# Kernel tuning notes

Hardware: AMD Instinct MI355X
Metric: run time of the kernel (lower is better)

The kernel has to match this reference:

```python
import jax, jax.numpy as jnp
import numpy as np

D = 512; H = 8; DK = 64; DFF = 512 * 8 // 3; NL = 3; WIN = 128
B = 4; L = 2048
VOCAB = 157; TE = 192


def _silu(x):
    return x * jax.nn.sigmoid(x)


def _ln(x, w, b):
    m = x.mean(-1, keepdims=True)
    v = ((x - m) ** 2).mean(-1, keepdims=True)
    return (x - m) / jnp.sqrt(v + 1e-5) * w + b


def _rms(x, w):
    return x / jnp.sqrt((x * x).mean(-1, keepdims=True) + 1.1920929e-7) * w


def _rope(t):
    # t: [B,H,L,DK]; rotary dim == DK (interleaved-pair convention of rotary-embedding-torch)
    Lq = t.shape[-2]
    inv = 1.0 / (10000.0 ** (jnp.arange(0, DK, 2, dtype=jnp.float32) / DK))
    ang = jnp.arange(Lq, dtype=jnp.float32)[:, None] * inv  # [L, DK/2]
    cos, sin = jnp.cos(ang), jnp.sin(ang)
    x1, x2 = t[..., ::2], t[..., 1::2]
    out = jnp.stack([x1 * cos - x2 * sin, x1 * sin + x2 * cos], axis=-1)
    return out.reshape(t.shape)


def _local_attn(h, qkv_w, ow, ob):
    Bq, Lq, _ = h.shape
    qkv = (h @ qkv_w.T).reshape(Bq, Lq, H, DK, 3)  # einops '(h d c)' ordering
    q = jnp.transpose(qkv[..., 0], (0, 2, 1, 3))
    k = jnp.transpose(qkv[..., 1], (0, 2, 1, 3))
    v = jnp.transpose(qkv[..., 2], (0, 2, 1, 3))
    q = _rope(q); k = _rope(k)
    nb = Lq // WIN
    qb = q.reshape(Bq, H, nb, WIN, DK)
    kb = k.reshape(Bq, H, nb, WIN, DK)
    vb = v.reshape(Bq, H, nb, WIN, DK)
    kp = jnp.concatenate([jnp.zeros_like(kb[:, :, :1]), kb[:, :, :-1]], axis=2)
    vp = jnp.concatenate([jnp.zeros_like(vb[:, :, :1]), vb[:, :, :-1]], axis=2)
    kc = jnp.concatenate([kp, kb], axis=3)  # [B,H,nb,2W,DK]
    vc = jnp.concatenate([vp, vb], axis=3)
    s = jnp.einsum('bhnqd,bhnkd->bhnqk', qb, kc) / np.float32(np.sqrt(DK))
    i = jnp.arange(WIN)[:, None]
    j = jnp.arange(2 * WIN)[None, :]
    band = (j >= i) & (j <= i + WIN)  # [W,2W]
    blk = jnp.arange(nb)[:, None, None]
    valid = band[None] & ((blk > 0) | (j[None] >= WIN))  # [nb,W,2W]
    s = jnp.where(valid[None, None], s, jnp.float32(-1e30))
    a = jax.nn.softmax(s, axis=-1)
    o = jnp.einsum('bhnqk,bhnkd->bhnqd', a, vc).reshape(Bq, H, Lq, DK)
    o = jnp.transpose(o, (0, 2, 1, 3)).reshape(Bq, Lq, D)
    return o @ ow.T + ob


def _net(x, emb, reg_w, reg_b, br_w, br_b, sh_w, sh_b, inst_w, inst_b, enc_ln_w, enc_ln_b,
         qkv_w, out_w, out_b, w1_w, w1_b, w3_w, w3_b, w2_w, w2_b, n1_w, n2_w,
         head_ln_w, head_ln_b, head_w, head_b):
    reg = x[..., 1:65].astype(jnp.float32)
    sh = x[..., 65:257].astype(jnp.float32)
    br = x[..., 257:289].astype(jnp.float32)
    te = emb[x[..., 0]]
    cat = jnp.concatenate([te, reg @ reg_w.T + reg_b, br @ br_w.T + br_b, sh @ sh_w.T + sh_b], axis=-1)
    h = _silu(cat) @ inst_w.T + inst_b
    h = _silu(_ln(h, enc_ln_w, enc_ln_b))
    for l in range(NL):
        h = h + _local_attn(_rms(h, n1_w[l]), qkv_w[l], out_w[l], out_b[l])
        h2 = _rms(h, n2_w[l])
        h = h + (_silu(h2 @ w1_w[l].T + w1_b[l]) * (h2 @ w3_w[l].T + w3_b[l])) @ w2_w[l].T + w2_b[l]
    y = _silu(_ln(h, head_ln_w, head_ln_b)) @ head_w.T + head_b  # [B,L,31]
    fc_log = y[..., 0:11]
    fc_reg = jax.nn.softplus(y[..., 11])
    ec_log = y[..., 12:23]
    ec_reg = jax.nn.softplus(y[..., 23])
    bm_log = y[..., 24]
    ic_log = y[..., 25:28]
    dc_log = y[..., 28:31]
    bm = jax.nn.sigmoid(bm_log)
    ic = jax.nn.softmax(ic_log, axis=-1)
    dc = jax.nn.softmax(dc_log, axis=-1)
    fc_pred = jnp.argmax(fc_log, axis=-1)
    fetch = jnp.where(fc_pred < 10, (fc_pred + 1).astype(jnp.float32), fc_reg)
    ec_pred = jnp.argmax(ec_log, axis=-1)
    execc = jnp.where(ec_pred < 10, (ec_pred + 1).astype(jnp.float32), ec_reg)
    # pack all task outputs into one [B,L,40] array
    return jnp.concatenate([
        fetch[..., None], fc_log, fc_reg[..., None],
        execc[..., None], ec_log, ec_reg[..., None],
        bm[..., None], ic, dc,
        bm_log[..., None], ic_log, dc_log], axis=-1)


def setup_inputs() -> dict:
    key = jax.random.key(0)
    ks = iter(jax.random.split(key, 64))
    g = lambda shape, s=0.02: (jax.random.normal(next(ks), shape, dtype=jnp.float32) * s)
    inp = {}
    inp['x'] = jax.random.randint(next(ks), (B, L, 289), 0, VOCAB, dtype=jnp.int64)
    inp['emb'] = g((VOCAB, TE), 1.0)
    inp['reg_w'] = g((TE, 64)); inp['reg_b'] = jnp.zeros((TE,), jnp.float32)
    inp['br_w'] = g((TE, 32)); inp['br_b'] = jnp.zeros((TE,), jnp.float32)
    inp['sh_w'] = g((TE, 192)); inp['sh_b'] = jnp.zeros((TE,), jnp.float32)
    inp['inst_w'] = g((D, 4 * TE)); inp['inst_b'] = jnp.zeros((D,), jnp.float32)
    inp['enc_ln_w'] = jnp.ones((D,), jnp.float32); inp['enc_ln_b'] = jnp.zeros((D,), jnp.float32)
    inp['qkv_w'] = g((NL, 3 * D, D))
    inp['out_w'] = g((NL, D, D)); inp['out_b'] = jnp.zeros((NL, D), jnp.float32)
    inp['w1_w'] = g((NL, DFF, D)); inp['w1_b'] = jnp.zeros((NL, DFF), jnp.float32)
    inp['w3_w'] = g((NL, DFF, D)); inp['w3_b'] = jnp.zeros((NL, DFF), jnp.float32)
    inp['w2_w'] = g((NL, D, DFF)); inp['w2_b'] = jnp.zeros((NL, D), jnp.float32)
    inp['n1_w'] = jnp.ones((NL, D), jnp.float32)
    inp['n2_w'] = jnp.ones((NL, D), jnp.float32)
    inp['head_ln_w'] = jnp.ones((D,), jnp.float32); inp['head_ln_b'] = jnp.zeros((D,), jnp.float32)
    inp['head_w'] = g((31, D)); inp['head_b'] = jnp.zeros((31,), jnp.float32)
    return inp


def reference(x, emb, reg_w, reg_b, br_w, br_b, sh_w, sh_b, inst_w, inst_b, enc_ln_w, enc_ln_b,
              qkv_w, out_w, out_b, w1_w, w1_b, w3_w, w3_b, w2_w, w2_b, n1_w, n2_w,
              head_ln_w, head_ln_b, head_w, head_b):
    return _net(x, emb, reg_w, reg_b, br_w, br_b, sh_w, sh_b, inst_w, inst_b, enc_ln_w, enc_ln_b,
                qkv_w, out_w, out_b, w1_w, w1_b, w3_w, w3_b, w2_w, w2_b, n1_w, n2_w,
                head_ln_w, head_ln_b, head_w, head_b)
```

## Files before the change

### kernel.cpp

```cpp
#include <hip/hip_runtime.h>
#include <hip/hip_bf16.h>
#include <math.h>

#define T_TOK 8192
#define DMODEL 512
#define NHEAD 8
#define TEDIM 192
#define DFF 1365
#define DFFP 1408
#define KP2 1376
#define NLAYER 3
#define WINSZ 128
#define NBLK 16
#define LSEQ 2048
#define BATCH 4

typedef unsigned short ushort_t;
typedef __bf16 bf16x8 __attribute__((ext_vector_type(8)));
typedef float f32x4 __attribute__((ext_vector_type(4)));
typedef float f32x16 __attribute__((ext_vector_type(16)));

__device__ __forceinline__ float silu_f(float x) { return x / (1.0f + expf(-x)); }
__device__ __forceinline__ float softplus_f(float x) {
    return (x > 20.0f) ? x : log1pf(expf(x));
}

__device__ __forceinline__ ushort_t f2u(float x) {
    __hip_bfloat16 b = __float2bfloat16(x);
    return *reinterpret_cast<ushort_t*>(&b);
}
__device__ __forceinline__ float u2f(ushort_t u) {
    __hip_bfloat16 b = *reinterpret_cast<__hip_bfloat16*>(&u);
    return __bfloat162float(b);
}
__device__ __forceinline__ void split2(float x, ushort_t& hi, ushort_t& lo) {
    hi = f2u(x);
    lo = f2u(x - u2f(hi));
}

__device__ __forceinline__ void gl_lds16(const ushort_t* g, ushort_t* l) {
    __builtin_amdgcn_global_load_lds(
        (const __attribute__((address_space(1))) unsigned int*)g,
        (__attribute__((address_space(3))) unsigned int*)l, 16, 0, 0);
}

__global__ __launch_bounds__(256)
void rope_kernel(float* __restrict__ ct, float* __restrict__ st) {
    int idx = blockIdx.x * 256 + threadIdx.x;
    int tok = idx >> 5, p = idx & 31;
    float invf = powf(10000.0f, -(float)p * (1.0f / 32.0f));
    float sn, cs;
    sincosf((float)tok * invf, &sn, &cs);
    ct[idx] = cs;
    st[idx] = sn;
}

__global__ __launch_bounds__(256)
void splitw_kernel(const float* __restrict__ W, ushort_t* __restrict__ W2,
                   int N, int K, int Kp) {
    int n = blockIdx.y;
    int k = blockIdx.x * 256 + threadIdx.x;
    if (k >= Kp) return;
    float v = (n < N && k < K) ? W[(size_t)n * K + k] : 0.0f;
    ushort_t hi, lo;
    split2(v, hi, lo);
    W2[(size_t)n * (2 * Kp) + k] = hi;
    W2[(size_t)n * (2 * Kp) + Kp + k] = lo;
}

__global__ __launch_bounds__(256)
void splitw_qkv_kernel(const float* __restrict__ W, ushort_t* __restrict__ W2) {
    int l = blockIdx.z;
    int rr = blockIdx.y;
    int k = blockIdx.x * 256 + threadIdx.x;
    int h = rr / 192, rem = rr % 192;
    int dk = rem / 3, which = rem % 3;
    int rp = which * 512 + h * 64 + dk;
    float v = W[((size_t)l * 1536 + rr) * 512 + k];
    ushort_t hi, lo;
    split2(v, hi, lo);
    W2[((size_t)l * 1536 + rp) * 1024 + k] = hi;
    W2[((size_t)l * 1536 + rp) * 1024 + 512 + k] = lo;
}

__global__ __launch_bounds__(256)
void splitw_ffn(const float* __restrict__ w1, const float* __restrict__ w3,
                ushort_t* __restrict__ W1s, ushort_t* __restrict__ W3s) {
    int rr = blockIdx.y;
    int k = blockIdx.x * 256 + threadIdx.x;
    int lyr = rr / DFFP, n = rr % DFFP;
    bool ok = (n < DFF);
    float v1 = ok ? w1[((size_t)lyr * DFF + n) * 512 + k] : 0.0f;
    float v3 = ok ? w3[((size_t)lyr * DFF + n) * 512 + k] : 0.0f;
    ushort_t hi, lo;
    split2(v1, hi, lo);
    W1s[(size_t)rr * 1024 + k] = hi;
    W1s[(size_t)rr * 1024 + 512 + k] = lo;
    split2(v3, hi, lo);
    W3s[(size_t)rr * 1024 + k] = hi;
    W3s[(size_t)rr * 1024 + 512 + k] = lo;
}

__global__ __launch_bounds__(256)
void splitw_w2(const float* __restrict__ W, ushort_t* __restrict__ W2) {
    int rr = blockIdx.y;
    int k = blockIdx.x * 256 + threadIdx.x;
    if (k >= KP2) return;
    int lyr = rr >> 9, n = rr & 511;
    float v = (k < DFF) ? W[((size_t)lyr * 512 + n) * DFF + k] : 0.0f;
    ushort_t hi, lo;
    split2(v, hi, lo);
    W2[(size_t)rr * (2 * KP2) + k] = hi;
    W2[(size_t)rr * (2 * KP2) + KP2 + k] = lo;
}

__global__ __launch_bounds__(256)
void build_encw(const float* __restrict__ reg_w, const float* __restrict__ reg_b,
                const float* __restrict__ br_w, const float* __restrict__ br_b,
                const float* __restrict__ sh_w, const float* __restrict__ sh_b,
                ushort_t* __restrict__ Wc2, float* __restrict__ bc) {
    int n = blockIdx.x;
    int tid = threadIdx.x;
    for (int k = tid; k < 288; k += 256) {
        float v = 0.0f;
        if (n < 192) {
            if (k < 64) v = reg_w[(size_t)n * 64 + k];
        } else if (n < 384) {
            if (k >= 256) v = br_w[(size_t)(n - 192) * 32 + (k - 256)];
        } else if (n < 576) {
            if (k >= 64 && k < 256) v = sh_w[(size_t)(n - 384) * 192 + (k - 64)];
        }
        ushort_t hi, lo;
        split2(v, hi, lo);
        Wc2[(size_t)n * 576 + k] = hi;
        Wc2[(size_t)n * 576 + 288 + k] = lo;
    }
    if (tid == 0) {
        float b = 0.0f;
        if (n < 192) b = reg_b[n];
        else if (n < 384) b = br_b[n - 192];
        else if (n < 576) b = sh_b[n - 384];
        bc[n] = b;
    }
}

__global__ __launch_bounds__(256)
void prep_tok(const int* __restrict__ x, const float* __restrict__ emb,
              ushort_t* __restrict__ X2, ushort_t* __restrict__ cat2) {
    int tok = blockIdx.x;
    int tid = threadIdx.x;
    const int* xp = x + (size_t)tok * 289;
    for (int k = tid; k < 288; k += 256) {
        X2[(size_t)tok * 576 + k] = f2u((float)xp[1 + k]);
        X2[(size_t)tok * 576 + 288 + k] = 0;
    }
    int tokid = xp[0];
    for (int c = tid; c < 192; c += 256) {
        float v = silu_f(emb[(size_t)tokid * TEDIM + c]);
        ushort_t hi, lo;
        split2(v, hi, lo);
        cat2[(size_t)tok * 1536 + c] = hi;
        cat2[(size_t)tok * 1536 + 768 + c] = lo;
    }
}


#define MFMA32(a, b, c) __builtin_amdgcn_mfma_f32_32x32x16_bf16(a, b, c, 0, 0, 0)

__global__ __launch_bounds__(256)
void gemm3_kernel(const ushort_t* __restrict__ A2, int rsA,
                  const ushort_t* __restrict__ B2, int rsB,
                  const float* __restrict__ bias,
                  const float* __restrict__ res,
                  float* __restrict__ Cf, int rsC, int Kp) {
    __shared__ __align__(16) ushort_t lds[4 * 4096];
    const int tid = threadIdx.x;
    const int bm = blockIdx.x * 128, bn = blockIdx.y * 128;
    const int w = tid >> 6, l = tid & 63;
    const int wm = (w & 1) * 64, wn = (w >> 1) * 64;

    f32x16 acc[2][2];
    #pragma unroll
    for (int i = 0; i < 2; ++i)
        #pragma unroll
        for (int j = 0; j < 2; ++j)
            #pragma unroll
            for (int r = 0; r < 16; ++r) acc[i][j][r] = 0.0f;

    const int r0 = tid >> 2;
    const int k8 = (((tid & 3) - (tid >> 3)) & 3) * 8;
    const ushort_t* gA0 = A2 + (size_t)(bm + r0) * rsA + k8;
    const ushort_t* gA1 = A2 + (size_t)(bm + 64 + r0) * rsA + k8;
    const ushort_t* gB0 = B2 + (size_t)(bn + r0) * rsB + k8;
    const ushort_t* gB1 = B2 + (size_t)(bn + 64 + r0) * rsB + k8;
    ushort_t* l0 = lds + tid * 8;
    ushort_t* l1 = lds + 2048 + tid * 8;

    const int ar = l & 31, qh = l >> 5;

    for (int kt = 0; kt < Kp; kt += 32) {
        gl_lds16(gA0 + kt, l0);
        gl_lds16(gA1 + kt, l1);
        gl_lds16(gA0 + kt + Kp, l0 + 4096);
        gl_lds16(gA1 + kt + Kp, l1 + 4096);
        gl_lds16(gB0 + kt, l0 + 8192);
        gl_lds16(gB1 + kt, l1 + 8192);
        gl_lds16(gB0 + kt + Kp, l0 + 12288);
        gl_lds16(gB1 + kt + Kp, l1 + 12288);
        __syncthreads();

        #pragma unroll
        for (int kh = 0; kh < 2; ++kh) {
            const int kq = kh * 2 + qh;
            bf16x8 ah[2], al_[2], bh[2], bl[2];
            #pragma unroll
            for (int i = 0; i < 2; ++i) {
                int row = wm + i * 32 + ar;
                int ba = row * 32 + (((kq + (row >> 1)) & 3) * 8);
                ah[i]  = *(const bf16x8*)&lds[ba];
                al_[i] = *(const bf16x8*)&lds[4096 + ba];
            }
            #pragma unroll
            for (int j = 0; j < 2; ++j) {
                int row = wn + j * 32 + ar;
                int bb = row * 32 + (((kq + (row >> 1)) & 3) * 8);
                bh[j] = *(const bf16x8*)&lds[8192 + bb];
                bl[j] = *(const bf16x8*)&lds[12288 + bb];
            }
            #pragma unroll
            for (int i = 0; i < 2; ++i)
                #pragma unroll
                for (int j = 0; j < 2; ++j) {
                    acc[i][j] = MFMA32(ah[i], bh[j], acc[i][j]);
                    acc[i][j] = MFMA32(ah[i], bl[j], acc[i][j]);
                    acc[i][j] = MFMA32(al_[i], bh[j], acc[i][j]);
                }
        }
        __syncthreads();
    }

    const int ec = l & 31, rb = (l >> 5) * 4;
    #pragma unroll
    for (int i = 0; i < 2; ++i)
        #pragma unroll
        for (int j = 0; j < 2; ++j) {
            int gn = bn + wn + j * 32 + ec;
            float bv = bias ? bias[gn] : 0.0f;
            #pragma unroll
            for (int r = 0; r < 16; ++r) {
                int gm = bm + wm + i * 32 + rb + (r & 3) + 8 * (r >> 2);
                float v = acc[i][j][r] + bv;
                if (res) v += res[(size_t)gm * rsC + gn];
                Cf[(size_t)gm * rsC + gn] = v;
            }
        }
}

__global__ __launch_bounds__(256)
void gemm3_enc(const ushort_t* __restrict__ A2, const ushort_t* __restrict__ B2,
               const float* __restrict__ bc, ushort_t* __restrict__ cat2) {
    __shared__ __align__(16) ushort_t lds[4 * 4096];
    const int tid = threadIdx.x;
    const int bm = blockIdx.x * 128, bn = blockIdx.y * 128;
    const int w = tid >> 6, l = tid & 63;
    const int wm = (w & 1) * 64, wn = (w >> 1) * 64;
    const int Kp = 288;

    f32x16 acc[2][2];
    #pragma unroll
    for (int i = 0; i < 2; ++i)
        #pragma unroll
        for (int j = 0; j < 2; ++j)
            #pragma unroll
            for (int r = 0; r < 16; ++r) acc[i][j][r] = 0.0f;

    const int r0 = tid >> 2;
    const int k8 = (((tid & 3) - (tid >> 3)) & 3) * 8;
    const ushort_t* gA0 = A2 + (size_t)(bm + r0) * 576 + k8;
    const ushort_t* gA1 = A2 + (size_t)(bm + 64 + r0) * 576 + k8;
    const ushort_t* gB0 = B2 + (size_t)(bn + r0) * 576 + k8;
    const ushort_t* gB1 = B2 + (size_t)(bn + 64 + r0) * 576 + k8;
    ushort_t* l0 = lds + tid * 8;
    ushort_t* l1 = lds + 2048 + tid * 8;
    const int ar = l & 31, qh = l >> 5;

    for (int kt = 0; kt < Kp; kt += 32) {
        gl_lds16(gA0 + kt, l0);
        gl_lds16(gA1 + kt, l1);
        gl_lds16(gA0 + kt + Kp, l0 + 4096);
        gl_lds16(gA1 + kt + Kp, l1 + 4096);
        gl_lds16(gB0 + kt, l0 + 8192);
        gl_lds16(gB1 + kt, l1 + 8192);
        gl_lds16(gB0 + kt + Kp, l0 + 12288);
        gl_lds16(gB1 + kt + Kp, l1 + 12288);
        __syncthreads();
        #pragma unroll
        for (int kh = 0; kh < 2; ++kh) {
            const int kq = kh * 2 + qh;
            bf16x8 ah[2], al_[2], bh[2], bl[2];
            #pragma unroll
            for (int i = 0; i < 2; ++i) {
                int row = wm + i * 32 + ar;
                int ba = row * 32 + (((kq + (row >> 1)) & 3) * 8);
                ah[i]  = *(const bf16x8*)&lds[ba];
                al_[i] = *(const bf16x8*)&lds[4096 + ba];
            }
            #pragma unroll
            for (int j = 0; j < 2; ++j) {
                int row = wn + j * 32 + ar;
                int bb = row * 32 + (((kq + (row >> 1)) & 3) * 8);
                bh[j] = *(const bf16x8*)&lds[8192 + bb];
                bl[j] = *(const bf16x8*)&lds[12288 + bb];
            }
            #pragma unroll
            for (int i = 0; i < 2; ++i)
                #pragma unroll
                for (int j = 0; j < 2; ++j) {
                    acc[i][j] = MFMA32(ah[i], bh[j], acc[i][j]);
                    acc[i][j] = MFMA32(ah[i], bl[j], acc[i][j]);
                    acc[i][j] = MFMA32(al_[i], bh[j], acc[i][j]);
                }
        }
        __syncthreads();
    }

    const int ec = l & 31, rb = (l >> 5) * 4;
    #pragma unroll
    for (int i = 0; i < 2; ++i)
        #pragma unroll
        for (int j = 0; j < 2; ++j) {
            int gn = bn + wn + j * 32 + ec;
            if (gn < 576) {
                float bv = bc[gn];
                #pragma unroll
                for (int r = 0; r < 16; ++r) {
                    int gm = bm + wm + i * 32 + rb + (r & 3) + 8 * (r >> 2);
                    float v = silu_f(acc[i][j][r] + bv);
                    ushort_t hi, lo;
                    split2(v, hi, lo);
                    cat2[(size_t)gm * 1536 + 192 + gn] = hi;
                    cat2[(size_t)gm * 1536 + 960 + gn] = lo;
                }
            }
        }
}

__global__ __launch_bounds__(256)
void gemm_glu3(const ushort_t* __restrict__ A2,
               const ushort_t* __restrict__ W1, const ushort_t* __restrict__ W3,
               const float* __restrict__ b1, const float* __restrict__ b3,
               ushort_t* __restrict__ C2) {
    __shared__ __align__(16) ushort_t lds[6 * 4096];
    const int tid = threadIdx.x;
    const int bm = blockIdx.x * 128, bn = blockIdx.y * 128;
    const int w = tid >> 6, l = tid & 63;
    const int wm = (w & 1) * 64, wn = (w >> 1) * 64;
    const int Kp = 512;

    f32x16 acc1[2][2], acc3[2][2];
    #pragma unroll
    for (int i = 0; i < 2; ++i)
        #pragma unroll
        for (int j = 0; j < 2; ++j)
            #pragma unroll
            for (int r = 0; r < 16; ++r) { acc1[i][j][r] = 0.0f; acc3[i][j][r] = 0.0f; }

    const int r0 = tid >> 2;
    const int k8 = (((tid & 3) - (tid >> 3)) & 3) * 8;
    const ushort_t* gA0 = A2 + (size_t)(bm + r0) * 1024 + k8;
    const ushort_t* gA1 = A2 + (size_t)(bm + 64 + r0) * 1024 + k8;
    const ushort_t* g10 = W1 + (size_t)(bn + r0) * 1024 + k8;
    const ushort_t* g11 = W1 + (size_t)(bn + 64 + r0) * 1024 + k8;
    const ushort_t* g30 = W3 + (size_t)(bn + r0) * 1024 + k8;
    const ushort_t* g31 = W3 + (size_t)(bn + 64 + r0) * 1024 + k8;
    ushort_t* l0 = lds + tid * 8;
    ushort_t* l1 = lds + 2048 + tid * 8;
    const int ar = l & 31, qh = l >> 5;

    for (int kt = 0; kt < Kp; kt += 32) {
        gl_lds16(gA0 + kt, l0);
        gl_lds16(gA1 + kt, l1);
        gl_lds16(gA0 + kt + Kp, l0 + 4096);
        gl_lds16(gA1 + kt + Kp, l1 + 4096);
        gl_lds16(g10 + kt, l0 + 8192);
        gl_lds16(g11 + kt, l1 + 8192);
        gl_lds16(g10 + kt + Kp, l0 + 12288);
        gl_lds16(g11 + kt + Kp, l1 + 12288);
        gl_lds16(g30 + kt, l0 + 16384);
        gl_lds16(g31 + kt, l1 + 16384);
        gl_lds16(g30 + kt + Kp, l0 + 20480);
        gl_lds16(g31 + kt + Kp, l1 + 20480);
        __syncthreads();

        #pragma unroll
        for (int kh = 0; kh < 2; ++kh) {
            const int kq = kh * 2 + qh;
            bf16x8 ah[2], al_[2];
            #pragma unroll
            for (int i = 0; i < 2; ++i) {
                int row = wm + i * 32 + ar;
                int ba = row * 32 + (((kq + (row >> 1)) & 3) * 8);
                ah[i]  = *(const bf16x8*)&lds[ba];
                al_[i] = *(const bf16x8*)&lds[4096 + ba];
            }
            #pragma unroll
            for (int j = 0; j < 2; ++j) {
                int row = wn + j * 32 + ar;
                int bb = row * 32 + (((kq + (row >> 1)) & 3) * 8);
                bf16x8 w1h = *(const bf16x8*)&lds[8192 + bb];
                bf16x8 w1l = *(const bf16x8*)&lds[12288 + bb];
                bf16x8 w3h = *(const bf16x8*)&lds[16384 + bb];
                bf16x8 w3l = *(const bf16x8*)&lds[20480 + bb];
                #pragma unroll
                for (int i = 0; i < 2; ++i) {
                    acc1[i][j] = MFMA32(ah[i], w1h, acc1[i][j]);
                    acc1[i][j] = MFMA32(ah[i], w1l, acc1[i][j]);
                    acc1[i][j] = MFMA32(al_[i], w1h, acc1[i][j]);
                    acc3[i][j] = MFMA32(ah[i], w3h, acc3[i][j]);
                    acc3[i][j] = MFMA32(ah[i], w3l, acc3[i][j]);
                    acc3[i][j] = MFMA32(al_[i], w3h, acc3[i][j]);
                }
            }
        }
        __syncthreads();
    }

    const int ec = l & 31, rb = (l >> 5) * 4;
    #pragma unroll
    for (int i = 0; i < 2; ++i)
        #pragma unroll
        for (int j = 0; j < 2; ++j) {
            int gn = bn + wn + j * 32 + ec;
            if (gn < KP2) {
                float bv1 = (gn < DFF) ? b1[gn] : 0.0f;
                float bv3 = (gn < DFF) ? b3[gn] : 0.0f;
                #pragma unroll
                for (int r = 0; r < 16; ++r) {
                    int gm = bm + wm + i * 32 + rb + (r & 3) + 8 * (r >> 2);
                    float g = silu_f(acc1[i][j][r] + bv1) * (acc3[i][j][r] + bv3);
                    ushort_t hi, lo;
                    split2(g, hi, lo);
                    C2[(size_t)gm * (2 * KP2) + gn] = hi;
                    C2[(size_t)gm * (2 * KP2) + KP2 + gn] = lo;
                }
            }
        }
}

__global__ __launch_bounds__(256)
void rms_kernel(const float* __restrict__ h, const float* __restrict__ w,
                ushort_t* __restrict__ out2) {
    int wid = threadIdx.x >> 6, lane = threadIdx.x & 63;
    int t = blockIdx.x * 4 + wid;
    const float* hp = h + (size_t)t * 512;
    float xv[8];
    float ss = 0.0f;
    #pragma unroll
    for (int u = 0; u < 8; ++u) { xv[u] = hp[u * 64 + lane]; ss += xv[u] * xv[u]; }
    #pragma unroll
    for (int off = 32; off > 0; off >>= 1) ss += __shfl_xor(ss, off, 64);
    float inv = rsqrtf(ss * (1.0f / 512.0f) + 1.1920929e-07f);
    ushort_t* op = out2 + (size_t)t * 1024;
    #pragma unroll
    for (int u = 0; u < 8; ++u) {
        ushort_t hi, lo;
        split2(xv[u] * inv * w[u * 64 + lane], hi, lo);
        op[u * 64 + lane] = hi;
        op[512 + u * 64 + lane] = lo;
    }
}

__global__ __launch_bounds__(256)
void ln_silu_kernel(const float* __restrict__ h, const float* __restrict__ w,
                    const float* __restrict__ b, float* __restrict__ out) {
    int wid = threadIdx.x >> 6, lane = threadIdx.x & 63;
    int t = blockIdx.x * 4 + wid;
    const float* hp = h + (size_t)t * 512;
    float xv[8];
    float s = 0.0f;
    #pragma unroll
    for (int u = 0; u < 8; ++u) { xv[u] = hp[u * 64 + lane]; s += xv[u]; }
    #pragma unroll
    for (int off = 32; off > 0; off >>= 1) s += __shfl_xor(s, off, 64);
    float m = s * (1.0f / 512.0f);
    float v = 0.0f;
    #pragma unroll
    for (int u = 0; u < 8; ++u) { xv[u] -= m; v += xv[u] * xv[u]; }
    #pragma unroll
    for (int off = 32; off > 0; off >>= 1) v += __shfl_xor(v, off, 64);
    float inv = rsqrtf(v * (1.0f / 512.0f) + 1e-5f);
    float* op = out + (size_t)t * 512;
    #pragma unroll
    for (int u = 0; u < 8; ++u)
        op[u * 64 + lane] = silu_f(xv[u] * inv * w[u * 64 + lane] + b[u * 64 + lane]);
}

__global__ __launch_bounds__(256)
void attn_kernel(const float* __restrict__ qkv, const float* __restrict__ ct,
                 const float* __restrict__ st, ushort_t* __restrict__ attn2) {
    __shared__ __align__(16) ushort_t Khi[32 * 64], Klo[32 * 64];
    __shared__ __align__(16) ushort_t Vthi[64 * 32], Vtlo[64 * 32];
    __shared__ __align__(16) ushort_t Phi[128 * 32], Plo[128 * 32];
    const int nb = blockIdx.x, head = blockIdx.y, b = blockIdx.z;
    const int tid = threadIdx.x;
    const int w = tid >> 6, lane = tid & 63;
    const int quad = lane >> 4, lc = lane & 15;

    bf16x8 qhi[2][2], qlo[2][2];
    #pragma unroll
    for (int i = 0; i < 2; ++i) {
        int qtok = nb * 128 + w * 32 + i * 16 + lc;
        const float* qp = qkv + ((size_t)(b * LSEQ + qtok)) * 1536 + head * 64;
        #pragma unroll
        for (int s = 0; s < 2; ++s) {
            float4 a = *(const float4*)&qp[s * 32 + quad * 8];
            float4 bq = *(const float4*)&qp[s * 32 + quad * 8 + 4];
            float4 c4 = *(const float4*)&ct[qtok * 32 + s * 16 + quad * 4];
            float4 s4 = *(const float4*)&st[qtok * 32 + s * 16 + quad * 4];
            float e[8];
            e[0] = (a.x * c4.x - a.y * s4.x) * 0.125f;
            e[1] = (a.x * s4.x + a.y * c4.x) * 0.125f;
            e[2] = (a.z * c4.y - a.w * s4.y) * 0.125f;
            e[3] = (a.z * s4.y + a.w * c4.y) * 0.125f;
            e[4] = (bq.x * c4.z - bq.y * s4.z) * 0.125f;
            e[5] = (bq.x * s4.z + bq.y * c4.z) * 0.125f;
            e[6] = (bq.z * c4.w - bq.w * s4.w) * 0.125f;
            e[7] = (bq.z * s4.w + bq.w * c4.w) * 0.125f;
            union { bf16x8 v; ushort_t u[8]; } hh, ll;
            #pragma unroll
            for (int d = 0; d < 8; ++d) split2(e[d], hh.u[d], ll.u[d]);
            qhi[i][s] = hh.v;
            qlo[i][s] = ll.v;
        }
    }

    f32x4 acc[2][4];
    float mrun[2][4], lrun[2][4];
    #pragma unroll
    for (int i = 0; i < 2; ++i) {
        #pragma unroll
        for (int j = 0; j < 4; ++j) acc[i][j] = (f32x4){0.f, 0.f, 0.f, 0.f};
        #pragma unroll
        for (int r = 0; r < 4; ++r) { mrun[i][r] = -1e30f; lrun[i][r] = 0.0f; }
    }

    const int c0 = (nb == 0) ? 4 : 0;
    for (int c = c0; c < 8; ++c) {
        {
            int key = tid >> 3, g = tid & 7;
            int ktok = nb * 128 - 128 + c * 32 + key;
            const float* kp = qkv + ((size_t)(b * LSEQ + ktok)) * 1536 + 512 + head * 64 + g * 8;
            float4 a = *(const float4*)kp;
            float4 bq = *(const float4*)(kp + 4);
            float4 c4 = *(const float4*)&ct[ktok * 32 + g * 4];
            float4 s4 = *(const float4*)&st[ktok * 32 + g * 4];
            float e[8];
            e[0] = a.x * c4.x - a.y * s4.x;
            e[1] = a.x * s4.x + a.y * c4.x;
            e[2] = a.z * c4.y - a.w * s4.y;
            e[3] = a.z * s4.y + a.w * c4.y;
            e[4] = bq.x * c4.z - bq.y * s4.z;
            e[5] = bq.x * s4.z + bq.y * c4.z;
            e[6] = bq.z * c4.w - bq.w * s4.w;
            e[7] = bq.z * s4.w + bq.w * c4.w;
            union { bf16x8 v; ushort_t u[8]; } hh, ll;
            #pragma unroll
            for (int d = 0; d < 8; ++d) split2(e[d], hh.u[d], ll.u[d]);
            int sg = g ^ (key & 7);
            *(bf16x8*)&Khi[key * 64 + sg * 8] = hh.v;
            *(bf16x8*)&Klo[key * 64 + sg * 8] = ll.v;

            const float* vp = kp + 512;
            float4 va = *(const float4*)vp;
            float4 vb = *(const float4*)(vp + 4);
            float ve[8] = {va.x, va.y, va.z, va.w, vb.x, vb.y, vb.z, vb.w};
            int kg = key >> 3, k7 = key & 7;
            #pragma unroll
            for (int d = 0; d < 8; ++d) {
                ushort_t vh, vl;
                split2(ve[d], vh, vl);
                int dim = g * 8 + d;
                int addr = dim * 32 + (((kg + (dim >> 1)) & 3) * 8) + k7;
                Vthi[addr] = vh;
                Vtlo[addr] = vl;
            }
        }
        __syncthreads();

        f32x4 sf[2][2];
        #pragma unroll
        for (int i = 0; i < 2; ++i)
            #pragma unroll
            for (int t = 0; t < 2; ++t) sf[i][t] = (f32x4){0.f, 0.f, 0.f, 0.f};
        #pragma unroll
        for (int t = 0; t < 2; ++t) {
            #pragma unroll
            for (int s = 0; s < 2; ++s) {
                int row = t * 16 + lc;
                int sg = (s * 4 + quad) ^ (row & 7);
                bf16x8 kh = *(const bf16x8*)&Khi[row * 64 + sg * 8];
                bf16x8 kl = *(const bf16x8*)&Klo[row * 64 + sg * 8];
                #pragma unroll
                for (int i = 0; i < 2; ++i) {
                    sf[i][t] = __builtin_amdgcn_mfma_f32_16x16x32_bf16(qhi[i][s], kh, sf[i][t], 0, 0, 0);
                    sf[i][t] = __builtin_amdgcn_mfma_f32_16x16x32_bf16(qhi[i][s], kl, sf[i][t], 0, 0, 0);
                    sf[i][t] = __builtin_amdgcn_mfma_f32_16x16x32_bf16(qlo[i][s], kh, sf[i][t], 0, 0, 0);
                }
            }
        }

        #pragma unroll
        for (int i = 0; i < 2; ++i) {
            #pragma unroll
            for (int r = 0; r < 4; ++r) {
                int qq = w * 32 + i * 16 + quad * 4 + r;
                float rm = -1e30f;
                #pragma unroll
                for (int t = 0; t < 2; ++t) {
                    int key = c * 32 + t * 16 + lc;
                    bool valid = (key >= qq) && (key <= qq + 128) && (nb > 0 || key >= 128);
                    float sv = valid ? sf[i][t][r] : -1e30f;
                    sf[i][t][r] = sv;
                    rm = fmaxf(rm, sv);
                }
                #pragma unroll
                for (int xm = 1; xm < 16; xm <<= 1)
                    rm = fmaxf(rm, __shfl_xor(rm, xm, 64));
                float mn = fmaxf(mrun[i][r], rm);
                float alpha = __expf(mrun[i][r] - mn);
                lrun[i][r] *= alpha;
                #pragma unroll
                for (int j = 0; j < 4; ++j) acc[i][j][r] *= alpha;
                float rs = 0.0f;
                #pragma unroll
                for (int t = 0; t < 2; ++t) {
                    int key = c * 32 + t * 16 + lc;
                    bool valid = (key >= qq) && (key <= qq + 128) && (nb > 0 || key >= 128);
                    float p = valid ? __expf(sf[i][t][r] - mn) : 0.0f;
                    rs += p;
                    ushort_t ph, pl;
                    split2(p, ph, pl);
                    int col = t * 16 + lc;
                    int addr = qq * 32 + ((((col >> 3) + (qq >> 1)) & 3) * 8) + (col & 7);
                    Phi[addr] = ph;
                    Plo[addr] = pl;
                }
                #pragma unroll
                for (int xm = 1; xm < 16; xm <<= 1)
                    rs += __shfl_xor(rs, xm, 64);
                lrun[i][r] += rs;
                mrun[i][r] = mn;
            }
        }

        bf16x8 ph[2], pl[2];
        #pragma unroll
        for (int i = 0; i < 2; ++i) {
            int row = w * 32 + i * 16 + lc;
            int sg = (quad + (row >> 1)) & 3;
            ph[i] = *(const bf16x8*)&Phi[row * 32 + sg * 8];
            pl[i] = *(const bf16x8*)&Plo[row * 32 + sg * 8];
        }
        #pragma unroll
        for (int j = 0; j < 4; ++j) {
            int dim = j * 16 + lc;
            int sg = (quad + (dim >> 1)) & 3;
            bf16x8 vh = *(const bf16x8*)&Vthi[dim * 32 + sg * 8];
            bf16x8 vl = *(const bf16x8*)&Vtlo[dim * 32 + sg * 8];
            #pragma unroll
            for (int i = 0; i < 2; ++i) {
                acc[i][j] = __builtin_amdgcn_mfma_f32_16x16x32_bf16(ph[i], vh, acc[i][j], 0, 0, 0);
                acc[i][j] = __builtin_amdgcn_mfma_f32_16x16x32_bf16(ph[i], vl, acc[i][j], 0, 0, 0);
                acc[i][j] = __builtin_amdgcn_mfma_f32_16x16x32_bf16(pl[i], vh, acc[i][j], 0, 0, 0);
            }
        }
        __syncthreads();
    }

    #pragma unroll
    for (int i = 0; i < 2; ++i) {
        #pragma unroll
        for (int r = 0; r < 4; ++r) {
            int qtok = nb * 128 + w * 32 + i * 16 + quad * 4 + r;
            size_t base = ((size_t)(b * LSEQ + qtok)) * 1024 + head * 64;
            float inv = 1.0f / lrun[i][r];
            #pragma unroll
            for (int j = 0; j < 4; ++j) {
                float v = acc[i][j][r] * inv;
                ushort_t hi, lo;
                split2(v, hi, lo);
                attn2[base + j * 16 + lc] = hi;
                attn2[base + 512 + j * 16 + lc] = lo;
            }
        }
    }
}

__global__ __launch_bounds__(256)
void head_kernel(const float* __restrict__ h, const float* __restrict__ lw,
                 const float* __restrict__ lb, const float* __restrict__ head_w,
                 const float* __restrict__ head_b, float* __restrict__ out) {
    int wid = threadIdx.x >> 6, lane = threadIdx.x & 63;
    int t = blockIdx.x * 4 + wid;
    __shared__ float yv[4][32];
    const float* xr = h + (size_t)t * 512;
    float xv[8];
    float s = 0.0f;
    #pragma unroll
    for (int u = 0; u < 8; ++u) { xv[u] = xr[u * 64 + lane]; s += xv[u]; }
    #pragma unroll
    for (int off = 32; off > 0; off >>= 1) s += __shfl_xor(s, off, 64);
    float m = s * (1.0f / 512.0f);
    float var = 0.0f;
    #pragma unroll
    for (int u = 0; u < 8; ++u) { xv[u] -= m; var += xv[u] * xv[u]; }
    #pragma unroll
    for (int off = 32; off > 0; off >>= 1) var += __shfl_xor(var, off, 64);
    float inv = rsqrtf(var * (1.0f / 512.0f) + 1e-5f);
    #pragma unroll
    for (int u = 0; u < 8; ++u)
        xv[u] = silu_f(xv[u] * inv * lw[u * 64 + lane] + lb[u * 64 + lane]);

    for (int j = 0; j < 31; ++j) {
        const float* wr = head_w + (size_t)j * 512;
        float p = 0.0f;
        #pragma unroll
        for (int u = 0; u < 8; ++u) p += xv[u] * wr[u * 64 + lane];
        #pragma unroll
        for (int off = 32; off > 0; off >>= 1) p += __shfl_down(p, off, 64);
        if (lane == 0) yv[wid][j] = p + head_b[j];
    }
    if (lane == 0) {
        float* y = yv[wid];
        float* op = out + (size_t)t * 40;
        int am = 0; float best = y[0];
        for (int j = 1; j < 11; ++j) if (y[j] > best) { best = y[j]; am = j; }
        float fc_reg = softplus_f(y[11]);
        op[0] = (am < 10) ? (float)(am + 1) : fc_reg;
        for (int j = 0; j < 11; ++j) op[1 + j] = y[j];
        op[12] = fc_reg;
        int am2 = 0; float best2 = y[12];
        for (int j = 1; j < 11; ++j) if (y[12 + j] > best2) { best2 = y[12 + j]; am2 = j; }
        float ec_reg = softplus_f(y[23]);
        op[13] = (am2 < 10) ? (float)(am2 + 1) : ec_reg;
        for (int j = 0; j < 11; ++j) op[14 + j] = y[12 + j];
        op[25] = ec_reg;
        float bm_log = y[24];
        op[26] = 1.0f / (1.0f + expf(-bm_log));
        float mi = fmaxf(y[25], fmaxf(y[26], y[27]));
        float e0 = expf(y[25] - mi), e1 = expf(y[26] - mi), e2 = expf(y[27] - mi);
        float si = e0 + e1 + e2;
        op[27] = e0 / si; op[28] = e1 / si; op[29] = e2 / si;
        float md = fmaxf(y[28], fmaxf(y[29], y[30]));
        float d0 = expf(y[28] - md), d1 = expf(y[29] - md), d2 = expf(y[30] - md);
        float sd = d0 + d1 + d2;
        op[30] = d0 / sd; op[31] = d1 / sd; op[32] = d2 / sd;
        op[33] = bm_log;
        op[34] = y[25]; op[35] = y[26]; op[36] = y[27];
        op[37] = y[28]; op[38] = y[29]; op[39] = y[30];
    }
}

extern "C" void kernel_launch(void* const* d_in, const int* in_sizes, int n_in,
                              void* d_out, int out_size, void* d_ws, size_t ws_size,
                              hipStream_t stream) {
    const int*   x        = (const int*)d_in[0];
    const float* emb      = (const float*)d_in[1];
    const float* reg_w    = (const float*)d_in[2];
    const float* reg_b    = (const float*)d_in[3];
    const float* br_w     = (const float*)d_in[4];
    const float* br_b     = (const float*)d_in[5];
    const float* sh_w     = (const float*)d_in[6];
    const float* sh_b     = (const float*)d_in[7];
    const float* inst_w   = (const float*)d_in[8];
    const float* inst_b   = (const float*)d_in[9];
    const float* enc_ln_w = (const float*)d_in[10];
    const float* enc_ln_b = (const float*)d_in[11];
    const float* qkv_w    = (const float*)d_in[12];
    const float* out_w    = (const float*)d_in[13];
    const float* out_b    = (const float*)d_in[14];
    const float* w1_w     = (const float*)d_in[15];
    const float* w1_b     = (const float*)d_in[16];
    const float* w3_w     = (const float*)d_in[17];
    const float* w3_b     = (const float*)d_in[18];
    const float* w2_w     = (const float*)d_in[19];
    const float* w2_b     = (const float*)d_in[20];
    const float* n1_w     = (const float*)d_in[21];
    const float* n2_w     = (const float*)d_in[22];
    const float* hl_w     = (const float*)d_in[23];
    const float* hl_b     = (const float*)d_in[24];
    const float* head_w   = (const float*)d_in[25];
    const float* head_b   = (const float*)d_in[26];

    char* ws = (char*)d_ws;
    size_t off = 0;
    ushort_t* inst2 = (ushort_t*)(ws + off); off += (size_t)512 * 1536 * 2;
    ushort_t* qkv2  = (ushort_t*)(ws + off); off += (size_t)3 * 1536 * 1024 * 2;
    ushort_t* out2w = (ushort_t*)(ws + off); off += (size_t)3 * 512 * 1024 * 2;
    ushort_t* w1s   = (ushort_t*)(ws + off); off += (size_t)3 * DFFP * 1024 * 2;
    ushort_t* w3s   = (ushort_t*)(ws + off); off += (size_t)3 * DFFP * 1024 * 2;
    ushort_t* w2s   = (ushort_t*)(ws + off); off += (size_t)3 * 512 * (2 * KP2) * 2;
    float*    ct    = (float*)(ws + off);    off += (size_t)LSEQ * 32 * 4;
    float*    st    = (float*)(ws + off);    off += (size_t)LSEQ * 32 * 4;
    float*    h     = (float*)(ws + off);    off += (size_t)T_TOK * 512 * 4;
    ushort_t* x2    = (ushort_t*)(ws + off); off += (size_t)T_TOK * 1024 * 2;
    ushort_t* attn2 = (ushort_t*)(ws + off); off += (size_t)T_TOK * 1024 * 2;
    float*    qkvb  = (float*)(ws + off);    off += (size_t)T_TOK * 1536 * 4;
    ushort_t* cat2  = (ushort_t*)(ws + off); off += (size_t)T_TOK * (2 * KP2) * 2;
    ushort_t* Wc2   = (ushort_t*)(ws + off); off += (size_t)640 * 576 * 2;
    float*    bc    = (float*)(ws + off);    off += 640 * 4;
    ushort_t* g2    = cat2;
    ushort_t* X2    = (ushort_t*)qkvb;

    rope_kernel<<<256, 256, 0, stream>>>(ct, st);
    build_encw<<<640, 256, 0, stream>>>(reg_w, reg_b, br_w, br_b, sh_w, sh_b, Wc2, bc);
    prep_tok<<<T_TOK, 256, 0, stream>>>(x, emb, X2, cat2);
    splitw_kernel<<<dim3(3, 512), 256, 0, stream>>>(inst_w, inst2, 512, 768, 768);
    splitw_qkv_kernel<<<dim3(2, 1536, 3), 256, 0, stream>>>(qkv_w, qkv2);
    splitw_kernel<<<dim3(2, 3 * 512), 256, 0, stream>>>(out_w, out2w, 3 * 512, 512, 512);
    splitw_ffn<<<dim3(2, 3 * DFFP), 256, 0, stream>>>(w1_w, w3_w, w1s, w3s);
    splitw_w2<<<dim3(6, 3 * 512), 256, 0, stream>>>(w2_w, w2s);

    gemm3_enc<<<dim3(64, 5), 256, 0, stream>>>(X2, Wc2, bc, cat2);
    gemm3_kernel<<<dim3(64, 4), 256, 0, stream>>>(
        cat2, 1536, inst2, 1536, inst_b, nullptr, h, 512, 768);
    ln_silu_kernel<<<T_TOK / 4, 256, 0, stream>>>(h, enc_ln_w, enc_ln_b, h);

    for (int l = 0; l < NLAYER; ++l) {
        rms_kernel<<<T_TOK / 4, 256, 0, stream>>>(h, n1_w + l * 512, x2);
        gemm3_kernel<<<dim3(64, 12), 256, 0, stream>>>(
            x2, 1024, qkv2 + (size_t)l * 1536 * 1024, 1024, nullptr, nullptr,
            qkvb, 1536, 512);
        {
            dim3 g(NBLK, NHEAD, BATCH);
            attn_kernel<<<g, 256, 0, stream>>>(qkvb, ct, st, attn2);
        }
        gemm3_kernel<<<dim3(64, 4), 256, 0, stream>>>(
            attn2, 1024, out2w + (size_t)l * 512 * 1024, 1024, out_b + l * 512,
            h, h, 512, 512);
        rms_kernel<<<T_TOK / 4, 256, 0, stream>>>(h, n2_w + l * 512, x2);
        gemm_glu3<<<dim3(64, 11), 256, 0, stream>>>(
            x2, w1s + (size_t)l * DFFP * 1024, w3s + (size_t)l * DFFP * 1024,
            w1_b + l * DFF, w3_b + l * DFF, g2);
        gemm3_kernel<<<dim3(64, 4), 256, 0, stream>>>(
            g2, 2 * KP2, w2s + (size_t)l * 512 * (2 * KP2), 2 * KP2, w2_b + l * 512,
            h, h, 512, KP2);
    }

    head_kernel<<<T_TOK / 4, 256, 0, stream>>>(h, hl_w, hl_b, head_w, head_b,
                                               (float*)d_out);
}
```

Before: 1.278 ms.

## Use 128x64 GEMM tiles for N=512 projections and trim encoder GEMM work

Adds a 128x64-tile split-bf16 GEMM and uses it for the inst, out-proj and W2 projections (N=512). This doubles the grid from 256 to 512 workgroups so the GPU's compute units are better filled. The encoder GEMM also drops the all-zero lo part of the integer input, cutting one MFMA per step and the A-side loads, and moves to 64-wide N tiles. The rope and encoder-weight setup kernels are merged into one launch. In exchange, each 64-wide tile reloads the A tile twice as often and gets less reuse per load.

```diff
diff --git a/kernel.cpp b/kernel.cpp
--- a/kernel.cpp
+++ b/kernel.cpp
@@ -45,14 +45,45 @@
 }
 
 __global__ __launch_bounds__(256)
-void rope_kernel(float* __restrict__ ct, float* __restrict__ st) {
-    int idx = blockIdx.x * 256 + threadIdx.x;
-    int tok = idx >> 5, p = idx & 31;
-    float invf = powf(10000.0f, -(float)p * (1.0f / 32.0f));
-    float sn, cs;
-    sincosf((float)tok * invf, &sn, &cs);
-    ct[idx] = cs;
-    st[idx] = sn;
+void prep_const(float* __restrict__ ct, float* __restrict__ st,
+                const float* __restrict__ reg_w, const float* __restrict__ reg_b,
+                const float* __restrict__ br_w, const float* __restrict__ br_b,
+                const float* __restrict__ sh_w, const float* __restrict__ sh_b,
+                ushort_t* __restrict__ Wc2, float* __restrict__ bc) {
+    int bx = blockIdx.x;
+    int tid = threadIdx.x;
+    if (bx < 256) {
+        int idx = bx * 256 + tid;
+        int tok = idx >> 5, p = idx & 31;
+        float invf = powf(10000.0f, -(float)p * (1.0f / 32.0f));
+        float sn, cs;
+        sincosf((float)tok * invf, &sn, &cs);
+        ct[idx] = cs;
+        st[idx] = sn;
+        return;
+    }
+    int n = bx - 256;
+    for (int k = tid; k < 288; k += 256) {
+        float v = 0.0f;
+        if (n < 192) {
+            if (k < 64) v = reg_w[(size_t)n * 64 + k];
+        } else if (n < 384) {
+            if (k >= 256) v = br_w[(size_t)(n - 192) * 32 + (k - 256)];
+        } else if (n < 576) {
+            if (k >= 64 && k < 256) v = sh_w[(size_t)(n - 384) * 192 + (k - 64)];
+        }
+        ushort_t hi, lo;
+        split2(v, hi, lo);
+        Wc2[(size_t)n * 576 + k] = hi;
+        Wc2[(size_t)n * 576 + 288 + k] = lo;
+    }
+    if (tid == 0) {
+        float b = 0.0f;
+        if (n < 192) b = reg_b[n];
+        else if (n < 384) b = br_b[n - 192];
+        else if (n < 576) b = sh_b[n - 384];
+        bc[n] = b;
+    }
 }
 
 __global__ __launch_bounds__(256)
@@ -115,45 +146,13 @@
 }
 
 __global__ __launch_bounds__(256)
-void build_encw(const float* __restrict__ reg_w, const float* __restrict__ reg_b,
-                const float* __restrict__ br_w, const float* __restrict__ br_b,
-                const float* __restrict__ sh_w, const float* __restrict__ sh_b,
-                ushort_t* __restrict__ Wc2, float* __restrict__ bc) {
-    int n = blockIdx.x;
-    int tid = threadIdx.x;
-    for (int k = tid; k < 288; k += 256) {
-        float v = 0.0f;
-        if (n < 192) {
-            if (k < 64) v = reg_w[(size_t)n * 64 + k];
-        } else if (n < 384) {
-            if (k >= 256) v = br_w[(size_t)(n - 192) * 32 + (k - 256)];
-        } else if (n < 576) {
-            if (k >= 64 && k < 256) v = sh_w[(size_t)(n - 384) * 192 + (k - 64)];
-        }
-        ushort_t hi, lo;
-        split2(v, hi, lo);
-        Wc2[(size_t)n * 576 + k] = hi;
-        Wc2[(size_t)n * 576 + 288 + k] = lo;
-    }
-    if (tid == 0) {
-        float b = 0.0f;
-        if (n < 192) b = reg_b[n];
-        else if (n < 384) b = br_b[n - 192];
-        else if (n < 576) b = sh_b[n - 384];
-        bc[n] = b;
-    }
-}
-
-__global__ __launch_bounds__(256)
 void prep_tok(const int* __restrict__ x, const float* __restrict__ emb,
               ushort_t* __restrict__ X2, ushort_t* __restrict__ cat2) {
     int tok = blockIdx.x;
     int tid = threadIdx.x;
     const int* xp = x + (size_t)tok * 289;
-    for (int k = tid; k < 288; k += 256) {
-        X2[(size_t)tok * 576 + k] = f2u((float)xp[1 + k]);
-        X2[(size_t)tok * 576 + 288 + k] = 0;
-    }
+    for (int k = tid; k < 288; k += 256)
+        X2[(size_t)tok * 288 + k] = f2u((float)xp[1 + k]);
     int tokid = xp[0];
     for (int c = tid; c < 192; c += 256) {
         float v = silu_f(emb[(size_t)tokid * TEDIM + c]);
@@ -257,31 +256,31 @@
 }
 
 __global__ __launch_bounds__(256)
-void gemm3_enc(const ushort_t* __restrict__ A2, const ushort_t* __restrict__ B2,
-               const float* __restrict__ bc, ushort_t* __restrict__ cat2) {
-    __shared__ __align__(16) ushort_t lds[4 * 4096];
+void gemm3_n64(const ushort_t* __restrict__ A2, int rsA,
+               const ushort_t* __restrict__ B2, int rsB,
+               const float* __restrict__ bias,
+               const float* __restrict__ res,
+               float* __restrict__ Cf, int rsC, int Kp) {
+    __shared__ __align__(16) ushort_t lds[12288];
     const int tid = threadIdx.x;
-    const int bm = blockIdx.x * 128, bn = blockIdx.y * 128;
+    const int bm = blockIdx.x * 128, bn = blockIdx.y * 64;
     const int w = tid >> 6, l = tid & 63;
-    const int wm = (w & 1) * 64, wn = (w >> 1) * 64;
-    const int Kp = 288;
-
-    f32x16 acc[2][2];
+    const int wm = (w & 1) * 64, wn = (w >> 1) * 32;
+
+    f32x16 acc[2];
     #pragma unroll
     for (int i = 0; i < 2; ++i)
         #pragma unroll
-        for (int j = 0; j < 2; ++j)
-            #pragma unroll
-            for (int r = 0; r < 16; ++r) acc[i][j][r] = 0.0f;
+        for (int r = 0; r < 16; ++r) acc[i][r] = 0.0f;
 
     const int r0 = tid >> 2;
     const int k8 = (((tid & 3) - (tid >> 3)) & 3) * 8;
-    const ushort_t* gA0 = A2 + (size_t)(bm + r0) * 576 + k8;
-    const ushort_t* gA1 = A2 + (size_t)(bm + 64 + r0) * 576 + k8;
-    const ushort_t* gB0 = B2 + (size_t)(bn + r0) * 576 + k8;
-    const ushort_t* gB1 = B2 + (size_t)(bn + 64 + r0) * 576 + k8;
+    const ushort_t* gA0 = A2 + (size_t)(bm + r0) * rsA + k8;
+    const ushort_t* gA1 = A2 + (size_t)(bm + 64 + r0) * rsA + k8;
+    const ushort_t* gB0 = B2 + (size_t)(bn + r0) * rsB + k8;
     ushort_t* l0 = lds + tid * 8;
     ushort_t* l1 = lds + 2048 + tid * 8;
+
     const int ar = l & 31, qh = l >> 5;
 
     for (int kt = 0; kt < Kp; kt += 32) {
@@ -290,14 +289,13 @@
         gl_lds16(gA0 + kt + Kp, l0 + 4096);
         gl_lds16(gA1 + kt + Kp, l1 + 4096);
         gl_lds16(gB0 + kt, l0 + 8192);
-        gl_lds16(gB1 + kt, l1 + 8192);
-        gl_lds16(gB0 + kt + Kp, l0 + 12288);
-        gl_lds16(gB1 + kt + Kp, l1 + 12288);
+        gl_lds16(gB0 + kt + Kp, l0 + 10240);
         __syncthreads();
+
         #pragma unroll
         for (int kh = 0; kh < 2; ++kh) {
             const int kq = kh * 2 + qh;
-            bf16x8 ah[2], al_[2], bh[2], bl[2];
+            bf16x8 ah[2], al_[2];
             #pragma unroll
             for (int i = 0; i < 2; ++i) {
                 int row = wm + i * 32 + ar;
@@ -305,44 +303,104 @@
                 ah[i]  = *(const bf16x8*)&lds[ba];
                 al_[i] = *(const bf16x8*)&lds[4096 + ba];
             }
-            #pragma unroll
-            for (int j = 0; j < 2; ++j) {
-                int row = wn + j * 32 + ar;
-                int bb = row * 32 + (((kq + (row >> 1)) & 3) * 8);
-                bh[j] = *(const bf16x8*)&lds[8192 + bb];
-                bl[j] = *(const bf16x8*)&lds[12288 + bb];
-            }
-            #pragma unroll
-            for (int i = 0; i < 2; ++i)
-                #pragma unroll
-                for (int j = 0; j < 2; ++j) {
-                    acc[i][j] = MFMA32(ah[i], bh[j], acc[i][j]);
-                    acc[i][j] = MFMA32(ah[i], bl[j], acc[i][j]);
-                    acc[i][j] = MFMA32(al_[i], bh[j], acc[i][j]);
-                }
+            int rowb = wn + ar;
+            int bb = rowb * 32 + (((kq + (rowb >> 1)) & 3) * 8);
+            bf16x8 bh = *(const bf16x8*)&lds[8192 + bb];
+            bf16x8 bl = *(const bf16x8*)&lds[10240 + bb];
+            #pragma unroll
+            for (int i = 0; i < 2; ++i) {
+                acc[i] = MFMA32(ah[i], bh, acc[i]);
+                acc[i] = MFMA32(ah[i], bl, acc[i]);
+                acc[i] = MFMA32(al_[i], bh, acc[i]);
+            }
         }
         __syncthreads();
     }
 
     const int ec = l & 31, rb = (l >> 5) * 4;
+    int gn = bn + wn + ec;
+    float bv = bias ? bias[gn] : 0.0f;
     #pragma unroll
     for (int i = 0; i < 2; ++i)
         #pragma unroll
-        for (int j = 0; j < 2; ++j) {
-            int gn = bn + wn + j * 32 + ec;
-            if (gn < 576) {
-                float bv = bc[gn];
-                #pragma unroll
-                for (int r = 0; r < 16; ++r) {
-                    int gm = bm + wm + i * 32 + rb + (r & 3) + 8 * (r >> 2);
-                    float v = silu_f(acc[i][j][r] + bv);
-                    ushort_t hi, lo;
-                    split2(v, hi, lo);
-                    cat2[(size_t)gm * 1536 + 192 + gn] = hi;
-                    cat2[(size_t)gm * 1536 + 960 + gn] = lo;
-                }
-            }
-        }
+        for (int r = 0; r < 16; ++r) {
+            int gm = bm + wm + i * 32 + rb + (r & 3) + 8 * (r >> 2);
+            float v = acc[i][r] + bv;
+            if (res) v += res[(size_t)gm * rsC + gn];
+            Cf[(size_t)gm * rsC + gn] = v;
+        }
+}
+
+__global__ __launch_bounds__(256)
+void gemm3_enc(const ushort_t* __restrict__ A2, const ushort_t* __restrict__ B2,
+               const float* __restrict__ bc, ushort_t* __restrict__ cat2) {
+    __shared__ __align__(16) ushort_t lds[8192];
+    const int tid = threadIdx.x;
+    const int bm = blockIdx.x * 128, bn = blockIdx.y * 64;
+    const int w = tid >> 6, l = tid & 63;
+    const int wm = (w & 1) * 64, wn = (w >> 1) * 32;
+    const int Kp = 288;
+
+    f32x16 acc[2];
+    #pragma unroll
+    for (int i = 0; i < 2; ++i)
+        #pragma unroll
+        for (int r = 0; r < 16; ++r) acc[i][r] = 0.0f;
+
+    const int r0 = tid >> 2;
+    const int k8 = (((tid & 3) - (tid >> 3)) & 3) * 8;
+    const ushort_t* gA0 = A2 + (size_t)(bm + r0) * 288 + k8;
+    const ushort_t* gA1 = A2 + (size_t)(bm + 64 + r0) * 288 + k8;
+    const ushort_t* gB0 = B2 + (size_t)(bn + r0) * 576 + k8;
+    ushort_t* l0 = lds + tid * 8;
+    ushort_t* l1 = lds + 2048 + tid * 8;
+    const int ar = l & 31, qh = l >> 5;
+
+    for (int kt = 0; kt < Kp; kt += 32) {
+        gl_lds16(gA0 + kt, l0);
+        gl_lds16(gA1 + kt, l1);
+        gl_lds16(gB0 + kt, l0 + 4096);
+        gl_lds16(gB0 + kt + Kp, l0 + 6144);
+        __syncthreads();
+        #pragma unroll
+        for (int kh = 0; kh < 2; ++kh) {
+            const int kq = kh * 2 + qh;
+            bf16x8 ah[2];
+            #pragma unroll
+            for (int i = 0; i < 2; ++i) {
+                int row = wm + i * 32 + ar;
+                int ba = row * 32 + (((kq + (row >> 1)) & 3) * 8);
+                ah[i] = *(const bf16x8*)&lds[ba];
+            }
+            int rowb = wn + ar;
+            int bb = rowb * 32 + (((kq + (rowb >> 1)) & 3) * 8);
+            bf16x8 bh = *(const bf16x8*)&lds[4096 + bb];
+            bf16x8 bl = *(const bf16x8*)&lds[6144 + bb];
+            #pragma unroll
+            for (int i = 0; i < 2; ++i) {
+                acc[i] = MFMA32(ah[i], bh, acc[i]);
+                acc[i] = MFMA32(ah[i], bl, acc[i]);
+            }
+        }
+        __syncthreads();
+    }
+
+    const int ec = l & 31, rb = (l >> 5) * 4;
+    int gn = bn + wn + ec;
+    if (gn < 576) {
+        float bv = bc[gn];
+        #pragma unroll
+        for (int i = 0; i < 2; ++i)
+            #pragma unroll
+            for (int r = 0; r < 16; ++r) {
+                int gm = bm + wm + i * 32 + rb + (r & 3) + 8 * (r >> 2);
+                float v = silu_f(acc[i][r] + bv);
+                ushort_t hi, lo;
+                split2(v, hi, lo);
+                cat2[(size_t)gm * 1536 + 192 + gn] = hi;
+                cat2[(size_t)gm * 1536 + 960 + gn] = lo;
+            }
+    }
 }
 
 __global__ __launch_bounds__(256)
@@ -812,8 +870,8 @@
     ushort_t* g2    = cat2;
     ushort_t* X2    = (ushort_t*)qkvb;
 
-    rope_kernel<<<256, 256, 0, stream>>>(ct, st);
-    build_encw<<<640, 256, 0, stream>>>(reg_w, reg_b, br_w, br_b, sh_w, sh_b, Wc2, bc);
+    prep_const<<<896, 256, 0, stream>>>(ct, st, reg_w, reg_b, br_w, br_b,
+                                        sh_w, sh_b, Wc2, bc);
     prep_tok<<<T_TOK, 256, 0, stream>>>(x, emb, X2, cat2);
     splitw_kernel<<<dim3(3, 512), 256, 0, stream>>>(inst_w, inst2, 512, 768, 768);
     splitw_qkv_kernel<<<dim3(2, 1536, 3), 256, 0, stream>>>(qkv_w, qkv2);
@@ -821,8 +879,8 @@
     splitw_ffn<<<dim3(2, 3 * DFFP), 256, 0, stream>>>(w1_w, w3_w, w1s, w3s);
     splitw_w2<<<dim3(6, 3 * 512), 256, 0, stream>>>(w2_w, w2s);
 
-    gemm3_enc<<<dim3(64, 5), 256, 0, stream>>>(X2, Wc2, bc, cat2);
-    gemm3_kernel<<<dim3(64, 4), 256, 0, stream>>>(
+    gemm3_enc<<<dim3(64, 10), 256, 0, stream>>>(X2, Wc2, bc, cat2);
+    gemm3_n64<<<dim3(64, 8), 256, 0, stream>>>(
         cat2, 1536, inst2, 1536, inst_b, nullptr, h, 512, 768);
     ln_silu_kernel<<<T_TOK / 4, 256, 0, stream>>>(h, enc_ln_w, enc_ln_b, h);
 
@@ -835,14 +893,14 @@
             dim3 g(NBLK, NHEAD, BATCH);
             attn_kernel<<<g, 256, 0, stream>>>(qkvb, ct, st, attn2);
         }
-        gemm3_kernel<<<dim3(64, 4), 256, 0, stream>>>(
+        gemm3_n64<<<dim3(64, 8), 256, 0, stream>>>(
             attn2, 1024, out2w + (size_t)l * 512 * 1024, 1024, out_b + l * 512,
             h, h, 512, 512);
         rms_kernel<<<T_TOK / 4, 256, 0, stream>>>(h, n2_w + l * 512, x2);
         gemm_glu3<<<dim3(64, 11), 256, 0, stream>>>(
             x2, w1s + (size_t)l * DFFP * 1024, w3s + (size_t)l * DFFP * 1024,
             w1_b + l * DFF, w3_b + l * DFF, g2);
-        gemm3_kernel<<<dim3(64, 4), 256, 0, stream>>>(
+        gemm3_n64<<<dim3(64, 8), 256, 0, stream>>>(
             g2, 2 * KP2, w2s + (size_t)l * 512 * (2 * KP2), 2 * KP2, w2_b + l * 512,
             h, h, 512, KP2);
     }
```

New measurement: 1.168 ms. -8.6%, faster.
